# Kernel tuning notes

Hardware: AMD Instinct MI355X
Metric: run time of the kernel (lower is better)

The kernel has to match this reference:

```python
import jax, jax.numpy as jnp
import numpy as np

B = 8192          # sessions
DOCS = 10         # docs per session
NPS = 21          # nodes per session: 1 query + 10 docs + 10 titles
N = B * NPS       # 172032 total nodes
F_IN, F_HID, F_OUT = 171, 256, 128


def _gat_conv(x, src, dst, W, a_src, a_dst, bias, n_nodes):
    # PyG GATConv, heads=1, negative_slope=0.2, self-loops already appended.
    h = x @ W.T                                   # [N, F]
    e = jax.nn.leaky_relu(jnp.take(h @ a_src, src) + jnp.take(h @ a_dst, dst), 0.2)
    m = jax.ops.segment_max(e, dst, num_segments=n_nodes)
    ex = jnp.exp(e - m[dst])
    denom = jax.ops.segment_sum(ex, dst, num_segments=n_nodes)
    alpha = ex / denom[dst]                       # softmax over incoming edges
    out = jax.ops.segment_sum(h[src] * alpha[:, None], dst, num_segments=n_nodes)
    return out + bias


def setup_inputs() -> dict:
    key = jax.random.key(0)
    ks = jax.random.split(key, 20)
    # structured node ids: per session block [q, d0..d9, t0..t9]
    base = jnp.arange(B, dtype=jnp.int64) * NPS
    doc_id = base[:, None] + 1 + jnp.arange(DOCS, dtype=jnp.int64)   # [B,10]
    q = base                                                          # query node = doc_id[:,0]-1
    t = doc_id + DOCS                                                 # title node = doc+10
    qd_s = jnp.repeat(q, DOCS); qd_d = doc_id.reshape(-1)
    dt_s = doc_id.reshape(-1);  dt_d = t.reshape(-1)
    src = jnp.concatenate([qd_s, qd_d, dt_s, dt_d])
    dst = jnp.concatenate([qd_d, qd_s, dt_d, dt_s])
    edge_index = jnp.stack([src, dst])                                # [2, 327680]

    inp = {
        "i": 0,
        "x": jax.random.normal(ks[0], (N, F_IN), jnp.float32),
        "edge_index": edge_index,
        "doc_id": doc_id,
        "click": jax.random.randint(ks[1], (B,), 0, 2),
        "query": jax.random.randint(ks[2], (B,), 0, 6338),
        "docu": jax.random.randint(ks[3], (B, DOCS), 0, 56477),
        "title_id": jax.random.randint(ks[4], (B, DOCS), 0, 56363),
        # embedding tables
        "query_table": jax.random.normal(ks[5], (6338, 160), jnp.float32) * 0.02,
        "doc_table": jax.random.normal(ks[6], (56477, 160), jnp.float32) * 0.02,
        "title_table": jax.random.normal(ks[7], (56363, 160), jnp.float32) * 0.02,
        "pos_table": jax.random.normal(ks[8], (10, 1), jnp.float32) * 0.02,
        "click_table": jax.random.normal(ks[9], (2, 1), jnp.float32) * 0.02,
        # GATConv 1 (171 -> 256)
        "W1": jax.random.normal(ks[10], (F_HID, F_IN), jnp.float32) * (1.0 / np.sqrt(F_IN)),
        "a_src1": jax.random.normal(ks[11], (F_HID,), jnp.float32) * 0.1,
        "a_dst1": jax.random.normal(ks[12], (F_HID,), jnp.float32) * 0.1,
        "b1": jnp.zeros((F_HID,), jnp.float32),
        # GATConv 2 (256 -> 128)
        "W2": jax.random.normal(ks[13], (F_OUT, F_HID), jnp.float32) * (1.0 / np.sqrt(F_HID)),
        "a_src2": jax.random.normal(ks[14], (F_OUT,), jnp.float32) * 0.1,
        "a_dst2": jax.random.normal(ks[15], (F_OUT,), jnp.float32) * 0.1,
        "b2": jnp.zeros((F_OUT,), jnp.float32),
        # head linear (128 -> 1)
        "Wl": jax.random.normal(ks[16], (1, F_OUT), jnp.float32) * (1.0 / np.sqrt(F_OUT)),
        "bl": jnp.zeros((1,), jnp.float32),
    }
    return inp


def reference(i, x, edge_index, doc_id, click, query, docu, title_id,
              query_table, doc_table, title_table, pos_table, click_table,
              W1, a_src1, a_dst1, b1, W2, a_src2, a_dst2, b2, Wl, bl):
    n_nodes = x.shape[0]
    q_emb = query_table[query]          # [B,160]
    d_emb = doc_table[docu]             # [B,10,160]
    t_emb = title_table[title_id]       # [B,10,160]
    pos = pos_table[:, 0]               # [10]  (position_embedding of 0..9)
    clk = click_table[click, 0]         # [B]

    df = doc_id.reshape(-1)             # flat doc node ids [B*10]
    if i == 0:
        x = x.at[doc_id[:, 0] - 1, :160].set(q_emb)
        x = x.at[df, :160].set(d_emb.reshape(-1, 160))
        x = x.at[df, 160].set(jnp.broadcast_to(pos, doc_id.shape).reshape(-1))
        x = x.at[df, 161 + i].set(jnp.broadcast_to(clk[:, None], doc_id.shape).reshape(-1))
        x = x.at[df + 10, :160].set(t_emb.reshape(-1, 160))
    else:
        x = x.at[df, 161 + i].set(jnp.broadcast_to(clk[:, None], doc_id.shape).reshape(-1))

    # add self-loops (PyG GATConv default)
    loop = jnp.arange(n_nodes, dtype=edge_index.dtype)
    src = jnp.concatenate([edge_index[0], loop])
    dst = jnp.concatenate([edge_index[1], loop])

    y = _gat_conv(x, src, dst, W1, a_src1, a_dst1, b1, n_nodes)
    y = jax.nn.relu(y)                  # dropout is identity in eval mode
    hidden_state = _gat_conv(y, src, dst, W2, a_src2, a_dst2, b2, n_nodes)
    y = jax.nn.relu(hidden_state)
    y = jax.nn.sigmoid(y @ Wl.T + bl)   # [N,1]
    return (hidden_state, y, x[:, :171])
```

## Files before the change

### kernel.cpp

```cpp
#include <hip/hip_runtime.h>
#include <cstdint>

#define N_NODES 172032
#define BATCH   8192
#define NPS     21
#define F_IN    171
#define K1P     192
#define F_HID   256
#define F_OUT   128
#define SX_F    (NPS * F_IN)
#define SXP     172
#define SXB     (NPS * K1P)
#define SPB     3
#define NBLK    2731

typedef unsigned short u16;
typedef __attribute__((ext_vector_type(8))) short  bf16x8;
typedef __attribute__((ext_vector_type(4))) float  f32x4;

__device__ inline u16 f2bf(float f) {
    unsigned u = __float_as_uint(f);
    unsigned r = u + 0x7FFFu + ((u >> 16) & 1u);
    return (u16)(r >> 16);
}
__device__ inline float bf2f(u16 h) { return __uint_as_float(((unsigned)h) << 16); }
__device__ inline float lrelu(float v) { return v > 0.f ? v : 0.2f * v; }

__device__ inline int deg_of(int n)  { return n == 0 ? 11 : (n <= 10 ? 3 : 2); }
__device__ inline int edge_base(int n) { return n == 0 ? 0 : (n <= 10 ? 11 + 3*(n-1) : 41 + 2*(n-11)); }
__device__ inline int src_of(int n, int k) {
    if (n == 0)  return k < 10 ? k + 1 : 0;
    if (n <= 10) return k == 0 ? 0 : (k == 1 ? n + 10 : n);
    return k == 0 ? n - 10 : n;
}

__device__ inline float wave_red(float v) {
    for (int off = 32; off; off >>= 1) v += __shfl_down(v, off);
    return v;
}

__global__ __launch_bounds__(256) void build_x(const int* __restrict__ iptr, const float* __restrict__ x,
                        const int* __restrict__ click, const int* __restrict__ query,
                        const int* __restrict__ docu, const int* __restrict__ title_id,
                        const float* __restrict__ qtab, const float* __restrict__ dtab,
                        const float* __restrict__ ttab, const float* __restrict__ ptab,
                        const float* __restrict__ ctab,
                        const float* __restrict__ W1, const float* __restrict__ W2,
                        float* __restrict__ out_x, u16* __restrict__ xb,
                        u16* __restrict__ W1b, u16* __restrict__ W2b)
{
    if (blockIdx.x >= BATCH) {
        int id = (blockIdx.x - BATCH) * 256 + threadIdx.x;
        if (id < 256 * K1P) {
            int r = id / K1P, k = id - r * K1P;
            W1b[id] = (k < F_IN) ? f2bf(W1[r * F_IN + k]) : (u16)0;
        }
        if (id < 128 * 256) W2b[id] = f2bf(W2[id]);
        return;
    }

    __shared__ float sx[NPS * SXP];
    __shared__ int   dz[10], tz[10], s_q;
    __shared__ float s_clk;

    const int s   = blockIdx.x;
    const int tid = threadIdx.x;
    const int i   = iptr[0];
    const long xbase = (long)s * SX_F;

    if (tid < 10)       dz[tid]      = docu[s*10 + tid];
    else if (tid < 20)  tz[tid - 10] = title_id[s*10 + tid - 10];
    else if (tid == 20) s_q          = query[s];
    else if (tid == 21) s_clk        = ctab[click[s]];
    __syncthreads();

    if (i == 0) {
        for (int id = tid; id < NPS * 40; id += 256) {
            int p = id / 40, c4 = (id - p * 40) * 4;
            const float* src;
            if (p == 0)       src = qtab + (long)s_q * 160;
            else if (p <= 10) src = dtab + (long)dz[p-1] * 160;
            else              src = ttab + (long)tz[p-11] * 160;
            *(float4*)(sx + p * SXP + c4) = *(const float4*)(src + c4);
        }
        for (int id = tid; id < NPS * 11; id += 256) {
            int p = id / 11, c = 160 + (id - p * 11);
            float v;
            if (p >= 1 && p <= 10 && c == 160)      v = ptab[p - 1];
            else if (p >= 1 && p <= 10 && c == 161) v = s_clk;
            else                                     v = x[xbase + p * F_IN + c];
            sx[p * SXP + c] = v;
        }
    } else {
        for (int idx = tid; idx < SX_F; idx += 256) {
            int p = idx / F_IN;
            int c = idx - p * F_IN;
            float v = x[xbase + idx];
            if (p >= 1 && p <= 10 && c == 161 + i) v = s_clk;
            sx[p * SXP + c] = v;
        }
    }
    __syncthreads();

    {
        int r    = (int)(xbase & 3);
        int head = (4 - r) & 3;
        if (tid < head) {
            int p = tid / F_IN, c = tid - p * F_IN;
            out_x[xbase + tid] = sx[p * SXP + c];
        }
        int n4 = (SX_F - head) >> 2;
        for (int id = tid; id < n4; id += 256) {
            int o = head + id * 4;
            float4 v;
            {
                int p0 = o / F_IN, c0 = o - p0 * F_IN;
                v.x = sx[p0 * SXP + c0];
                int o1 = o + 1; int p1 = o1 / F_IN, c1 = o1 - p1 * F_IN;
                v.y = sx[p1 * SXP + c1];
                int o2 = o + 2; int p2 = o2 / F_IN, c2 = o2 - p2 * F_IN;
                v.z = sx[p2 * SXP + c2];
                int o3 = o + 3; int p3 = o3 / F_IN, c3 = o3 - p3 * F_IN;
                v.w = sx[p3 * SXP + c3];
            }
            *(float4*)(out_x + xbase + o) = v;
        }
        int done = head + n4 * 4;
        int tail = SX_F - done;
        if (tid < tail) {
            int idx = done + tid;
            int p = idx / F_IN, c = idx - p * F_IN;
            out_x[xbase + idx] = sx[p * SXP + c];
        }
    }

    {
        u16* xbs = xb + (long)s * SXB;
        for (int id = tid; id < SXB / 8; id += 256) {
            int k0 = id * 8;
            int node = k0 / K1P;
            int kk   = k0 - node * K1P;
            union { u16 h[8]; uint4 v; } u;
            #pragma unroll
            for (int j = 0; j < 8; ++j) {
                int c = kk + j;
                u.h[j] = (c < F_IN) ? f2bf(sx[node * SXP + c]) : (u16)0;
            }
            *(uint4*)(xbs + k0) = u.v;
        }
    }
}

__global__ __launch_bounds__(256, 4) void fused1(const u16* __restrict__ xb, const u16* __restrict__ W1b,
                                                 const float* __restrict__ asrc, const float* __restrict__ adst,
                                                 const float* __restrict__ bias, u16* __restrict__ y1b)
{
    constexpr int SA = 200;
    __shared__ __align__(16) u16 hbuf[64 * 256];
    __shared__ float s_part[2][64], d_part[2][64];
    __shared__ float alpha[SPB * 61];

    const int blk = blockIdx.x, tid = threadIdx.x;
    const int s0  = blk * SPB;
    const int nsamp = (s0 + SPB <= BATCH) ? SPB : (BATCH - s0);
    const int nrow  = nsamp * NPS;

    const int lane = tid & 63, w = tid >> 6;
    const int wr = w >> 1, wc = w & 1;
    const int lm = lane & 15, lq = lane >> 4;

    const u16* Ag = xb + (long)s0 * SXB;
    for (int id = tid; id < 64 * 24; id += 256) {
        int row = id / 24, ch = id - row * 24;
        uint4 v;
        if (row < nrow) v = *(const uint4*)(Ag + row * K1P + ch * 8);
        else            v = make_uint4(0u, 0u, 0u, 0u);
        *(uint4*)(hbuf + row * SA + ch * 8) = v;
    }
    __syncthreads();

    f32x4 acc[2][8];
    #pragma unroll
    for (int f = 0; f < 2; ++f)
        #pragma unroll
        for (int g = 0; g < 8; ++g)
            acc[f][g] = (f32x4){0.f, 0.f, 0.f, 0.f};

    #pragma unroll
    for (int kb = 0; kb < K1P / 32; ++kb) {
        int koff = kb * 32 + lq * 8;
        bf16x8 a0 = *(const bf16x8*)(hbuf + (wr*32 +  0 + lm) * SA + koff);
        bf16x8 a1 = *(const bf16x8*)(hbuf + (wr*32 + 16 + lm) * SA + koff);
        #pragma unroll
        for (int g = 0; g < 8; ++g) {
            bf16x8 b = *(const bf16x8*)(W1b + (wc*128 + g*16 + lm) * K1P + koff);
            acc[0][g] = __builtin_amdgcn_mfma_f32_16x16x32_bf16(a0, b, acc[0][g], 0, 0, 0);
            acc[1][g] = __builtin_amdgcn_mfma_f32_16x16x32_bf16(a1, b, acc[1][g], 0, 0, 0);
        }
    }
    __syncthreads();

    u16* h = hbuf;
    float av[8], dv[8];
    #pragma unroll
    for (int g = 0; g < 8; ++g) {
        av[g] = asrc[wc*128 + g*16 + lm];
        dv[g] = adst[wc*128 + g*16 + lm];
    }
    #pragma unroll
    for (int f = 0; f < 2; ++f)
        #pragma unroll
        for (int r = 0; r < 4; ++r) {
            int row = wr*32 + f*16 + lq*4 + r;
            float sp = 0.f, dp = 0.f;
            #pragma unroll
            for (int g = 0; g < 8; ++g) {
                float v = acc[f][g][r];
                h[row * F_HID + wc*128 + g*16 + lm] = f2bf(v);
                sp += v * av[g];
                dp += v * dv[g];
            }
            #pragma unroll
            for (int off = 1; off < 16; off <<= 1) {
                sp += __shfl_xor(sp, off);
                dp += __shfl_xor(dp, off);
            }
            if (lm == 0) { s_part[wc][row] = sp; d_part[wc][row] = dp; }
        }
    __syncthreads();

    if (tid < nrow) {
        int s = tid / NPS, p = tid - s * NPS;
        int deg = deg_of(p), eb = edge_base(p);
        int sb = s * NPS;
        float dn = d_part[0][tid] + d_part[1][tid];
        float e[11];
        float m = -1e30f;
        for (int k = 0; k < deg; ++k) {
            int sn = sb + src_of(p, k);
            e[k] = lrelu(s_part[0][sn] + s_part[1][sn] + dn);
            m = fmaxf(m, e[k]);
        }
        float den = 0.f;
        for (int k = 0; k < deg; ++k) { e[k] = expf(e[k] - m); den += e[k]; }
        float inv = 1.f / den;
        for (int k = 0; k < deg; ++k) alpha[s*61 + eb + k] = e[k] * inv;
    }
    __syncthreads();

    const int c = tid;
    float bc = bias[c];
    for (int s = 0; s < nsamp; ++s) {
        const u16* hs = h + s * NPS * F_HID;
        const float* al = alpha + s * 61;
        u16* outp = y1b + ((long)(s0 + s) * NPS) * F_HID;
        {
            float a = al[10] * bf2f(hs[c]);
            #pragma unroll
            for (int j = 1; j <= 10; ++j) a += al[j-1] * bf2f(hs[j * F_HID + c]);
            outp[c] = f2bf(fmaxf(a + bc, 0.f));
        }
        #pragma unroll
        for (int j = 1; j <= 10; ++j) {
            int eb = 11 + 3*(j-1);
            float a = al[eb]   * bf2f(hs[c])
                    + al[eb+1] * bf2f(hs[(j+10) * F_HID + c])
                    + al[eb+2] * bf2f(hs[j * F_HID + c]);
            outp[j * F_HID + c] = f2bf(fmaxf(a + bc, 0.f));
        }
        #pragma unroll
        for (int j = 1; j <= 10; ++j) {
            int eb = 41 + 2*(j-1);
            float a = al[eb]   * bf2f(hs[j * F_HID + c])
                    + al[eb+1] * bf2f(hs[(10+j) * F_HID + c]);
            outp[(10+j) * F_HID + c] = f2bf(fmaxf(a + bc, 0.f));
        }
    }
}

__global__ __launch_bounds__(256, 4) void fused2(const u16* __restrict__ y1b, const u16* __restrict__ W2b,
                                                 const float* __restrict__ asrc, const float* __restrict__ adst,
                                                 const float* __restrict__ bias,
                                                 const float* __restrict__ Wl, const float* __restrict__ bl,
                                                 float* __restrict__ out_hid, float* __restrict__ out_y)
{
    constexpr int SA = 264;
    __shared__ __align__(16) u16 hbuf[64 * SA];
    __shared__ float s_part[2][64], d_part[2][64];
    __shared__ float alpha[SPB * 61];
    __shared__ float rpart[SPB * NPS][2];

    const int blk = blockIdx.x, tid = threadIdx.x;
    const int s0  = blk * SPB;
    const int nsamp = (s0 + SPB <= BATCH) ? SPB : (BATCH - s0);
    const int nrow  = nsamp * NPS;

    const int lane = tid & 63, w = tid >> 6;
    const int wr = w >> 1, wc = w & 1;
    const int lm = lane & 15, lq = lane >> 4;

    const u16* Ag = y1b + (long)s0 * NPS * F_HID;
    for (int id = tid; id < 64 * 32; id += 256) {
        int row = id >> 5, ch = id & 31;
        uint4 v;
        if (row < nrow) v = *(const uint4*)(Ag + row * F_HID + ch * 8);
        else            v = make_uint4(0u, 0u, 0u, 0u);
        *(uint4*)(hbuf + row * SA + ch * 8) = v;
    }
    __syncthreads();

    f32x4 acc[2][4];
    #pragma unroll
    for (int f = 0; f < 2; ++f)
        #pragma unroll
        for (int g = 0; g < 4; ++g)
            acc[f][g] = (f32x4){0.f, 0.f, 0.f, 0.f};

    #pragma unroll
    for (int kb = 0; kb < F_HID / 32; ++kb) {
        int koff = kb * 32 + lq * 8;
        bf16x8 a0 = *(const bf16x8*)(hbuf + (wr*32 +  0 + lm) * SA + koff);
        bf16x8 a1 = *(const bf16x8*)(hbuf + (wr*32 + 16 + lm) * SA + koff);
        #pragma unroll
        for (int g = 0; g < 4; ++g) {
            bf16x8 b = *(const bf16x8*)(W2b + (wc*64 + g*16 + lm) * F_HID + koff);
            acc[0][g] = __builtin_amdgcn_mfma_f32_16x16x32_bf16(a0, b, acc[0][g], 0, 0, 0);
            acc[1][g] = __builtin_amdgcn_mfma_f32_16x16x32_bf16(a1, b, acc[1][g], 0, 0, 0);
        }
    }
    __syncthreads();

    u16* h2 = hbuf;
    float av[4], dv[4];
    #pragma unroll
    for (int g = 0; g < 4; ++g) {
        av[g] = asrc[wc*64 + g*16 + lm];
        dv[g] = adst[wc*64 + g*16 + lm];
    }
    #pragma unroll
    for (int f = 0; f < 2; ++f)
        #pragma unroll
        for (int r = 0; r < 4; ++r) {
            int row = wr*32 + f*16 + lq*4 + r;
            float sp = 0.f, dp = 0.f;
            #pragma unroll
            for (int g = 0; g < 4; ++g) {
                float v = acc[f][g][r];
                h2[row * F_OUT + wc*64 + g*16 + lm] = f2bf(v);
                sp += v * av[g];
                dp += v * dv[g];
            }
            #pragma unroll
            for (int off = 1; off < 16; off <<= 1) {
                sp += __shfl_xor(sp, off);
                dp += __shfl_xor(dp, off);
            }
            if (lm == 0) { s_part[wc][row] = sp; d_part[wc][row] = dp; }
        }
    __syncthreads();

    if (tid < nrow) {
        int s = tid / NPS, p = tid - s * NPS;
        int deg = deg_of(p), eb = edge_base(p);
        int sb = s * NPS;
        float dn = d_part[0][tid] + d_part[1][tid];
        float e[11];
        float m = -1e30f;
        for (int k = 0; k < deg; ++k) {
            int sn = sb + src_of(p, k);
            e[k] = lrelu(s_part[0][sn] + s_part[1][sn] + dn);
            m = fmaxf(m, e[k]);
        }
        float den = 0.f;
        for (int k = 0; k < deg; ++k) { e[k] = expf(e[k] - m); den += e[k]; }
        float inv = 1.f / den;
        for (int k = 0; k < deg; ++k) alpha[s*61 + eb + k] = e[k] * inv;
    }
    __syncthreads();

    const int c    = tid & 127;
    const int half = tid >> 7;
    float bc = bias[c];
    float wl = Wl[c];
    for (int s = 0; s < nsamp; ++s) {
        const u16* hs = h2 + s * NPS * F_OUT;
        const float* al = alpha + s * 61;
        long gb = (long)(s0 + s) * NPS * F_OUT;
        for (int p = half; p < NPS; p += 2) {
            int deg = deg_of(p), eb = edge_base(p);
            float a = 0.f;
            for (int k = 0; k < deg; ++k) a += al[eb + k] * bf2f(hs[src_of(p,k) * F_OUT + c]);
            float hv = a + bc;
            out_hid[gb + p * F_OUT + c] = hv;
            float rv = wave_red(fmaxf(hv, 0.f) * wl);
            if (lane == 0) rpart[s * NPS + p][w & 1] = rv;
        }
    }
    __syncthreads();

    if (tid < nrow) {
        float v = rpart[tid][0] + rpart[tid][1] + bl[0];
        out_y[(long)s0 * NPS + tid] = 1.f / (1.f + expf(-v));
    }
}

extern "C" void kernel_launch(void* const* d_in, const int* in_sizes, int n_in,
                              void* d_out, int out_size, void* d_ws, size_t ws_size,
                              hipStream_t stream) {
    const int*   ip    = (const int*)  d_in[0];
    const float* x     = (const float*)d_in[1];
    const int*   click = (const int*)  d_in[4];
    const int*   query = (const int*)  d_in[5];
    const int*   docu  = (const int*)  d_in[6];
    const int*   title = (const int*)  d_in[7];
    const float* qtab  = (const float*)d_in[8];
    const float* dtab  = (const float*)d_in[9];
    const float* ttab  = (const float*)d_in[10];
    const float* ptab  = (const float*)d_in[11];
    const float* ctab  = (const float*)d_in[12];
    const float* W1    = (const float*)d_in[13];
    const float* as1   = (const float*)d_in[14];
    const float* ad1   = (const float*)d_in[15];
    const float* b1    = (const float*)d_in[16];
    const float* W2    = (const float*)d_in[17];
    const float* as2   = (const float*)d_in[18];
    const float* ad2   = (const float*)d_in[19];
    const float* b2    = (const float*)d_in[20];
    const float* Wl    = (const float*)d_in[21];
    const float* bl    = (const float*)d_in[22];

    float* out_hid = (float*)d_out;
    float* out_y   = out_hid + (long)N_NODES * F_OUT;
    float* out_x   = out_y + N_NODES;

    u16* xb  = (u16*)d_ws;
    u16* y1b = xb + (long)BATCH * SXB;
    u16* W1b = y1b + (long)N_NODES * F_HID;
    u16* W2b = W1b + 256 * K1P;

    build_x<<<BATCH + 192, 256, 0, stream>>>(ip, x, click, query, docu, title,
                                             qtab, dtab, ttab, ptab, ctab,
                                             W1, W2, out_x, xb, W1b, W2b);
    fused1<<<NBLK, 256, 0, stream>>>(xb, W1b, as1, ad1, b1, y1b);
    fused2<<<NBLK, 256, 0, stream>>>(y1b, W2b, as2, ad2, b2, Wl, bl, out_hid, out_y);
}
```

Measured before the change: 571.1 us.

## Fuse input build and both GAT layers into one per-block kernel

Merges the build_x, fused1 and fused2 kernels into a single kernel that gathers embeddings, writes out_x, converts to bf16 in shared memory, and runs both GAT layers with intermediates kept in LDS. Weight conversion moves to a small separate kernel. This removes the global round trips for the bf16 x buffer and the 256-wide hidden activations, plus two launches. In exchange, LDS use per block rises (two large buffers), launch bounds drop to 2 blocks per CU, and the out_x writes become scalar strided stores instead of float4.

```diff
diff --git a/kernel.cpp b/kernel.cpp
--- a/kernel.cpp
+++ b/kernel.cpp
@@ -9,14 +9,13 @@
 #define F_HID   256
 #define F_OUT   128
 #define SX_F    (NPS * F_IN)
-#define SXP     172
-#define SXB     (NPS * K1P)
 #define SPB     3
 #define NBLK    2731
 
 typedef unsigned short u16;
 typedef __attribute__((ext_vector_type(8))) short  bf16x8;
 typedef __attribute__((ext_vector_type(4))) float  f32x4;
+typedef __attribute__((ext_vector_type(4))) u16    u16x4;
 
 __device__ inline u16 f2bf(float f) {
     unsigned u = __float_as_uint(f);
@@ -39,143 +38,101 @@
     return v;
 }
 
-__global__ __launch_bounds__(256) void build_x(const int* __restrict__ iptr, const float* __restrict__ x,
+__global__ __launch_bounds__(256) void prep_w(const float* __restrict__ W1, const float* __restrict__ W2,
+                                              u16* __restrict__ W1b, u16* __restrict__ W2b)
+{
+    int id = blockIdx.x * 256 + threadIdx.x;
+    if (id < 256 * K1P) {
+        int r = id / K1P, k = id - r * K1P;
+        W1b[id] = (k < F_IN) ? f2bf(W1[r * F_IN + k]) : (u16)0;
+    }
+    if (id < 128 * 256) W2b[id] = f2bf(W2[id]);
+}
+
+__global__ __launch_bounds__(256, 2) void mega(const int* __restrict__ iptr, const float* __restrict__ x,
                         const int* __restrict__ click, const int* __restrict__ query,
                         const int* __restrict__ docu, const int* __restrict__ title_id,
                         const float* __restrict__ qtab, const float* __restrict__ dtab,
                         const float* __restrict__ ttab, const float* __restrict__ ptab,
                         const float* __restrict__ ctab,
-                        const float* __restrict__ W1, const float* __restrict__ W2,
-                        float* __restrict__ out_x, u16* __restrict__ xb,
-                        u16* __restrict__ W1b, u16* __restrict__ W2b)
+                        const u16* __restrict__ W1b, const u16* __restrict__ W2b,
+                        const float* __restrict__ as1, const float* __restrict__ ad1,
+                        const float* __restrict__ b1,
+                        const float* __restrict__ as2, const float* __restrict__ ad2,
+                        const float* __restrict__ b2,
+                        const float* __restrict__ Wl, const float* __restrict__ bl,
+                        float* __restrict__ out_x, float* __restrict__ out_hid,
+                        float* __restrict__ out_y)
 {
-    if (blockIdx.x >= BATCH) {
-        int id = (blockIdx.x - BATCH) * 256 + threadIdx.x;
-        if (id < 256 * K1P) {
-            int r = id / K1P, k = id - r * K1P;
-            W1b[id] = (k < F_IN) ? f2bf(W1[r * F_IN + k]) : (u16)0;
-        }
-        if (id < 128 * 256) W2b[id] = f2bf(W2[id]);
-        return;
-    }
-
-    __shared__ float sx[NPS * SXP];
-    __shared__ int   dz[10], tz[10], s_q;
-    __shared__ float s_clk;
-
-    const int s   = blockIdx.x;
-    const int tid = threadIdx.x;
-    const int i   = iptr[0];
-    const long xbase = (long)s * SX_F;
-
-    if (tid < 10)       dz[tid]      = docu[s*10 + tid];
-    else if (tid < 20)  tz[tid - 10] = title_id[s*10 + tid - 10];
-    else if (tid == 20) s_q          = query[s];
-    else if (tid == 21) s_clk        = ctab[click[s]];
-    __syncthreads();
-
-    if (i == 0) {
-        for (int id = tid; id < NPS * 40; id += 256) {
-            int p = id / 40, c4 = (id - p * 40) * 4;
-            const float* src;
-            if (p == 0)       src = qtab + (long)s_q * 160;
-            else if (p <= 10) src = dtab + (long)dz[p-1] * 160;
-            else              src = ttab + (long)tz[p-11] * 160;
-            *(float4*)(sx + p * SXP + c4) = *(const float4*)(src + c4);
-        }
-        for (int id = tid; id < NPS * 11; id += 256) {
-            int p = id / 11, c = 160 + (id - p * 11);
-            float v;
-            if (p >= 1 && p <= 10 && c == 160)      v = ptab[p - 1];
-            else if (p >= 1 && p <= 10 && c == 161) v = s_clk;
-            else                                     v = x[xbase + p * F_IN + c];
-            sx[p * SXP + c] = v;
-        }
-    } else {
-        for (int idx = tid; idx < SX_F; idx += 256) {
-            int p = idx / F_IN;
-            int c = idx - p * F_IN;
-            float v = x[xbase + idx];
-            if (p >= 1 && p <= 10 && c == 161 + i) v = s_clk;
-            sx[p * SXP + c] = v;
-        }
-    }
-    __syncthreads();
-
-    {
-        int r    = (int)(xbase & 3);
-        int head = (4 - r) & 3;
-        if (tid < head) {
-            int p = tid / F_IN, c = tid - p * F_IN;
-            out_x[xbase + tid] = sx[p * SXP + c];
-        }
-        int n4 = (SX_F - head) >> 2;
-        for (int id = tid; id < n4; id += 256) {
-            int o = head + id * 4;
-            float4 v;
-            {
-                int p0 = o / F_IN, c0 = o - p0 * F_IN;
-                v.x = sx[p0 * SXP + c0];
-                int o1 = o + 1; int p1 = o1 / F_IN, c1 = o1 - p1 * F_IN;
-                v.y = sx[p1 * SXP + c1];
-                int o2 = o + 2; int p2 = o2 / F_IN, c2 = o2 - p2 * F_IN;
-                v.z = sx[p2 * SXP + c2];
-                int o3 = o + 3; int p3 = o3 / F_IN, c3 = o3 - p3 * F_IN;
-                v.w = sx[p3 * SXP + c3];
-            }
-            *(float4*)(out_x + xbase + o) = v;
-        }
-        int done = head + n4 * 4;
-        int tail = SX_F - done;
-        if (tid < tail) {
-            int idx = done + tid;
-            int p = idx / F_IN, c = idx - p * F_IN;
-            out_x[xbase + idx] = sx[p * SXP + c];
-        }
-    }
-
-    {
-        u16* xbs = xb + (long)s * SXB;
-        for (int id = tid; id < SXB / 8; id += 256) {
-            int k0 = id * 8;
-            int node = k0 / K1P;
-            int kk   = k0 - node * K1P;
-            union { u16 h[8]; uint4 v; } u;
-            #pragma unroll
-            for (int j = 0; j < 8; ++j) {
-                int c = kk + j;
-                u.h[j] = (c < F_IN) ? f2bf(sx[node * SXP + c]) : (u16)0;
-            }
-            *(uint4*)(xbs + k0) = u.v;
-        }
-    }
-}
-
-__global__ __launch_bounds__(256, 4) void fused1(const u16* __restrict__ xb, const u16* __restrict__ W1b,
-                                                 const float* __restrict__ asrc, const float* __restrict__ adst,
-                                                 const float* __restrict__ bias, u16* __restrict__ y1b)
-{
-    constexpr int SA = 200;
-    __shared__ __align__(16) u16 hbuf[64 * 256];
+    constexpr int SA1 = 200;
+    constexpr int SA2 = 264;
+    __shared__ __align__(16) u16 R2[64 * SA2];
+    __shared__ __align__(16) u16 R1[64 * F_HID];
     __shared__ float s_part[2][64], d_part[2][64];
     __shared__ float alpha[SPB * 61];
+    __shared__ float rpart[SPB * NPS][2];
+    __shared__ int   dz[SPB][10], tz[SPB][10], sq[SPB];
+    __shared__ float sclk[SPB];
 
     const int blk = blockIdx.x, tid = threadIdx.x;
     const int s0  = blk * SPB;
     const int nsamp = (s0 + SPB <= BATCH) ? SPB : (BATCH - s0);
     const int nrow  = nsamp * NPS;
+    const int i     = iptr[0];
 
     const int lane = tid & 63, w = tid >> 6;
     const int wr = w >> 1, wc = w & 1;
     const int lm = lane & 15, lq = lane >> 4;
 
-    const u16* Ag = xb + (long)s0 * SXB;
-    for (int id = tid; id < 64 * 24; id += 256) {
-        int row = id / 24, ch = id - row * 24;
-        uint4 v;
-        if (row < nrow) v = *(const uint4*)(Ag + row * K1P + ch * 8);
-        else            v = make_uint4(0u, 0u, 0u, 0u);
-        *(uint4*)(hbuf + row * SA + ch * 8) = v;
+    if (tid < 30)      { int ss = tid / 10, j = tid - ss*10;       if (ss < nsamp) dz[ss][j] = docu[(s0+ss)*10 + j]; }
+    else if (tid < 60) { int t = tid - 30; int ss = t/10, j = t - ss*10; if (ss < nsamp) tz[ss][j] = title_id[(s0+ss)*10 + j]; }
+    else if (tid >= 64 && tid < 67) { int ss = tid - 64; if (ss < nsamp) sq[ss]   = query[s0+ss]; }
+    else if (tid >= 67 && tid < 70) { int ss = tid - 67; if (ss < nsamp) sclk[ss] = ctab[click[s0+ss]]; }
+    __syncthreads();
+
+    u16* A1 = R2;
+    if (i == 0) {
+        for (int id = tid; id < nrow * 40; id += 256) {
+            int r = id / 40, c4 = (id - r*40) * 4;
+            int ss = r / NPS, p = r - ss*NPS;
+            const float* srcp;
+            if (p == 0)       srcp = qtab + (long)sq[ss] * 160;
+            else if (p <= 10) srcp = dtab + (long)dz[ss][p-1] * 160;
+            else              srcp = ttab + (long)tz[ss][p-11] * 160;
+            float4 v = *(const float4*)(srcp + c4);
+            float* ox = out_x + (long)(s0+ss) * SX_F + p * F_IN + c4;
+            ox[0] = v.x; ox[1] = v.y; ox[2] = v.z; ox[3] = v.w;
+            u16x4 hv = { f2bf(v.x), f2bf(v.y), f2bf(v.z), f2bf(v.w) };
+            *(u16x4*)(A1 + r * SA1 + c4) = hv;
+        }
+        for (int id = tid; id < nrow * 11; id += 256) {
+            int r = id / 11, c = 160 + (id - r*11);
+            int ss = r / NPS, p = r - ss*NPS;
+            float v;
+            if (p >= 1 && p <= 10 && c == 160)      v = ptab[p-1];
+            else if (p >= 1 && p <= 10 && c == 161) v = sclk[ss];
+            else v = x[(long)(s0+ss) * SX_F + p * F_IN + c];
+            out_x[(long)(s0+ss) * SX_F + p * F_IN + c] = v;
+            A1[r * SA1 + c] = f2bf(v);
+        }
+    } else {
+        const long base0 = (long)s0 * SX_F;
+        for (int idx = tid; idx < nrow * F_IN; idx += 256) {
+            int r = idx / F_IN, c = idx - r * F_IN;
+            int ss = r / NPS, p = r - ss*NPS;
+            float v = x[base0 + idx];
+            if (p >= 1 && p <= 10 && c == 161 + i) v = sclk[ss];
+            out_x[base0 + idx] = v;
+            A1[r * SA1 + c] = f2bf(v);
+        }
+    }
+    for (int id = tid; id < nrow * 21; id += 256) {
+        int r = id / 21, c = F_IN + (id - r*21);
+        A1[r * SA1 + c] = 0;
+    }
+    for (int id = tid; id < (64 - nrow) * 24; id += 256) {
+        int r = nrow + id / 24, ch = id - (id/24)*24;
+        *(uint4*)(A1 + r * SA1 + ch * 8) = make_uint4(0u,0u,0u,0u);
     }
     __syncthreads();
 
@@ -189,8 +146,8 @@
     #pragma unroll
     for (int kb = 0; kb < K1P / 32; ++kb) {
         int koff = kb * 32 + lq * 8;
-        bf16x8 a0 = *(const bf16x8*)(hbuf + (wr*32 +  0 + lm) * SA + koff);
-        bf16x8 a1 = *(const bf16x8*)(hbuf + (wr*32 + 16 + lm) * SA + koff);
+        bf16x8 a0 = *(const bf16x8*)(A1 + (wr*32 +  0 + lm) * SA1 + koff);
+        bf16x8 a1 = *(const bf16x8*)(A1 + (wr*32 + 16 + lm) * SA1 + koff);
         #pragma unroll
         for (int g = 0; g < 8; ++g) {
             bf16x8 b = *(const bf16x8*)(W1b + (wc*128 + g*16 + lm) * K1P + koff);
@@ -198,35 +155,36 @@
             acc[1][g] = __builtin_amdgcn_mfma_f32_16x16x32_bf16(a1, b, acc[1][g], 0, 0, 0);
         }
     }
-    __syncthreads();
-
-    u16* h = hbuf;
-    float av[8], dv[8];
-    #pragma unroll
-    for (int g = 0; g < 8; ++g) {
-        av[g] = asrc[wc*128 + g*16 + lm];
-        dv[g] = adst[wc*128 + g*16 + lm];
-    }
-    #pragma unroll
-    for (int f = 0; f < 2; ++f)
-        #pragma unroll
-        for (int r = 0; r < 4; ++r) {
-            int row = wr*32 + f*16 + lq*4 + r;
-            float sp = 0.f, dp = 0.f;
+
+    u16* h1 = R1;
+    {
+        float av[8], dv[8];
+        #pragma unroll
+        for (int g = 0; g < 8; ++g) {
+            av[g] = as1[wc*128 + g*16 + lm];
+            dv[g] = ad1[wc*128 + g*16 + lm];
+        }
+        #pragma unroll
+        for (int f = 0; f < 2; ++f)
             #pragma unroll
-            for (int g = 0; g < 8; ++g) {
-                float v = acc[f][g][r];
-                h[row * F_HID + wc*128 + g*16 + lm] = f2bf(v);
-                sp += v * av[g];
-                dp += v * dv[g];
-            }
-            #pragma unroll
-            for (int off = 1; off < 16; off <<= 1) {
-                sp += __shfl_xor(sp, off);
-                dp += __shfl_xor(dp, off);
-            }
-            if (lm == 0) { s_part[wc][row] = sp; d_part[wc][row] = dp; }
-        }
+            for (int r = 0; r < 4; ++r) {
+                int row = wr*32 + f*16 + lq*4 + r;
+                float sp = 0.f, dp = 0.f;
+                #pragma unroll
+                for (int g = 0; g < 8; ++g) {
+                    float v = acc[f][g][r];
+                    h1[row * F_HID + wc*128 + g*16 + lm] = f2bf(v);
+                    sp += v * av[g];
+                    dp += v * dv[g];
+                }
+                #pragma unroll
+                for (int off = 1; off < 16; off <<= 1) {
+                    sp += __shfl_xor(sp, off);
+                    dp += __shfl_xor(dp, off);
+                }
+                if (lm == 0) { s_part[wc][row] = sp; d_part[wc][row] = dp; }
+            }
+    }
     __syncthreads();
 
     if (tid < nrow) {
@@ -248,115 +206,88 @@
     }
     __syncthreads();
 
-    const int c = tid;
-    float bc = bias[c];
-    for (int s = 0; s < nsamp; ++s) {
-        const u16* hs = h + s * NPS * F_HID;
-        const float* al = alpha + s * 61;
-        u16* outp = y1b + ((long)(s0 + s) * NPS) * F_HID;
-        {
-            float a = al[10] * bf2f(hs[c]);
+    u16* Y = R2;
+    {
+        const int c = tid;
+        float bc = b1[c];
+        for (int s = 0; s < nsamp; ++s) {
+            const u16* hs = h1 + s * NPS * F_HID;
+            const float* al = alpha + s * 61;
+            u16* yrow = Y + (s * NPS) * SA2;
+            {
+                float a = al[10] * bf2f(hs[c]);
+                #pragma unroll
+                for (int j = 1; j <= 10; ++j) a += al[j-1] * bf2f(hs[j * F_HID + c]);
+                yrow[c] = f2bf(fmaxf(a + bc, 0.f));
+            }
             #pragma unroll
-            for (int j = 1; j <= 10; ++j) a += al[j-1] * bf2f(hs[j * F_HID + c]);
-            outp[c] = f2bf(fmaxf(a + bc, 0.f));
-        }
-        #pragma unroll
-        for (int j = 1; j <= 10; ++j) {
-            int eb = 11 + 3*(j-1);
-            float a = al[eb]   * bf2f(hs[c])
-                    + al[eb+1] * bf2f(hs[(j+10) * F_HID + c])
-                    + al[eb+2] * bf2f(hs[j * F_HID + c]);
-            outp[j * F_HID + c] = f2bf(fmaxf(a + bc, 0.f));
-        }
-        #pragma unroll
-        for (int j = 1; j <= 10; ++j) {
-            int eb = 41 + 2*(j-1);
-            float a = al[eb]   * bf2f(hs[j * F_HID + c])
-                    + al[eb+1] * bf2f(hs[(10+j) * F_HID + c]);
-            outp[(10+j) * F_HID + c] = f2bf(fmaxf(a + bc, 0.f));
-        }
-    }
-}
-
-__global__ __launch_bounds__(256, 4) void fused2(const u16* __restrict__ y1b, const u16* __restrict__ W2b,
-                                                 const float* __restrict__ asrc, const float* __restrict__ adst,
-                                                 const float* __restrict__ bias,
-                                                 const float* __restrict__ Wl, const float* __restrict__ bl,
-                                                 float* __restrict__ out_hid, float* __restrict__ out_y)
-{
-    constexpr int SA = 264;
-    __shared__ __align__(16) u16 hbuf[64 * SA];
-    __shared__ float s_part[2][64], d_part[2][64];
-    __shared__ float alpha[SPB * 61];
-    __shared__ float rpart[SPB * NPS][2];
-
-    const int blk = blockIdx.x, tid = threadIdx.x;
-    const int s0  = blk * SPB;
-    const int nsamp = (s0 + SPB <= BATCH) ? SPB : (BATCH - s0);
-    const int nrow  = nsamp * NPS;
-
-    const int lane = tid & 63, w = tid >> 6;
-    const int wr = w >> 1, wc = w & 1;
-    const int lm = lane & 15, lq = lane >> 4;
-
-    const u16* Ag = y1b + (long)s0 * NPS * F_HID;
-    for (int id = tid; id < 64 * 32; id += 256) {
-        int row = id >> 5, ch = id & 31;
-        uint4 v;
-        if (row < nrow) v = *(const uint4*)(Ag + row * F_HID + ch * 8);
-        else            v = make_uint4(0u, 0u, 0u, 0u);
-        *(uint4*)(hbuf + row * SA + ch * 8) = v;
-    }
-    __syncthreads();
-
-    f32x4 acc[2][4];
+            for (int j = 1; j <= 10; ++j) {
+                int eb = 11 + 3*(j-1);
+                float a = al[eb]   * bf2f(hs[c])
+                        + al[eb+1] * bf2f(hs[(j+10) * F_HID + c])
+                        + al[eb+2] * bf2f(hs[j * F_HID + c]);
+                yrow[j * SA2 + c] = f2bf(fmaxf(a + bc, 0.f));
+            }
+            #pragma unroll
+            for (int j = 1; j <= 10; ++j) {
+                int eb = 41 + 2*(j-1);
+                float a = al[eb]   * bf2f(hs[j * F_HID + c])
+                        + al[eb+1] * bf2f(hs[(10+j) * F_HID + c]);
+                yrow[(10+j) * SA2 + c] = f2bf(fmaxf(a + bc, 0.f));
+            }
+        }
+    }
+    __syncthreads();
+
+    f32x4 acc2[2][4];
     #pragma unroll
     for (int f = 0; f < 2; ++f)
         #pragma unroll
         for (int g = 0; g < 4; ++g)
-            acc[f][g] = (f32x4){0.f, 0.f, 0.f, 0.f};
+            acc2[f][g] = (f32x4){0.f, 0.f, 0.f, 0.f};
 
     #pragma unroll
     for (int kb = 0; kb < F_HID / 32; ++kb) {
         int koff = kb * 32 + lq * 8;
-        bf16x8 a0 = *(const bf16x8*)(hbuf + (wr*32 +  0 + lm) * SA + koff);
-        bf16x8 a1 = *(const bf16x8*)(hbuf + (wr*32 + 16 + lm) * SA + koff);
+        bf16x8 a0 = *(const bf16x8*)(Y + (wr*32 +  0 + lm) * SA2 + koff);
+        bf16x8 a1 = *(const bf16x8*)(Y + (wr*32 + 16 + lm) * SA2 + koff);
         #pragma unroll
         for (int g = 0; g < 4; ++g) {
             bf16x8 b = *(const bf16x8*)(W2b + (wc*64 + g*16 + lm) * F_HID + koff);
-            acc[0][g] = __builtin_amdgcn_mfma_f32_16x16x32_bf16(a0, b, acc[0][g], 0, 0, 0);
-            acc[1][g] = __builtin_amdgcn_mfma_f32_16x16x32_bf16(a1, b, acc[1][g], 0, 0, 0);
-        }
-    }
-    __syncthreads();
-
-    u16* h2 = hbuf;
-    float av[4], dv[4];
-    #pragma unroll
-    for (int g = 0; g < 4; ++g) {
-        av[g] = asrc[wc*64 + g*16 + lm];
-        dv[g] = adst[wc*64 + g*16 + lm];
-    }
-    #pragma unroll
-    for (int f = 0; f < 2; ++f)
-        #pragma unroll
-        for (int r = 0; r < 4; ++r) {
-            int row = wr*32 + f*16 + lq*4 + r;
-            float sp = 0.f, dp = 0.f;
+            acc2[0][g] = __builtin_amdgcn_mfma_f32_16x16x32_bf16(a0, b, acc2[0][g], 0, 0, 0);
+            acc2[1][g] = __builtin_amdgcn_mfma_f32_16x16x32_bf16(a1, b, acc2[1][g], 0, 0, 0);
+        }
+    }
+
+    u16* h2 = R1;
+    {
+        float av[4], dv[4];
+        #pragma unroll
+        for (int g = 0; g < 4; ++g) {
+            av[g] = as2[wc*64 + g*16 + lm];
+            dv[g] = ad2[wc*64 + g*16 + lm];
+        }
+        #pragma unroll
+        for (int f = 0; f < 2; ++f)
             #pragma unroll
-            for (int g = 0; g < 4; ++g) {
-                float v = acc[f][g][r];
-                h2[row * F_OUT + wc*64 + g*16 + lm] = f2bf(v);
-                sp += v * av[g];
-                dp += v * dv[g];
-            }
-            #pragma unroll
-            for (int off = 1; off < 16; off <<= 1) {
-                sp += __shfl_xor(sp, off);
-                dp += __shfl_xor(dp, off);
-            }
-            if (lm == 0) { s_part[wc][row] = sp; d_part[wc][row] = dp; }
-        }
+            for (int r = 0; r < 4; ++r) {
+                int row = wr*32 + f*16 + lq*4 + r;
+                float sp = 0.f, dp = 0.f;
+                #pragma unroll
+                for (int g = 0; g < 4; ++g) {
+                    float v = acc2[f][g][r];
+                    h2[row * F_OUT + wc*64 + g*16 + lm] = f2bf(v);
+                    sp += v * av[g];
+                    dp += v * dv[g];
+                }
+                #pragma unroll
+                for (int off = 1; off < 16; off <<= 1) {
+                    sp += __shfl_xor(sp, off);
+                    dp += __shfl_xor(dp, off);
+                }
+                if (lm == 0) { s_part[wc][row] = sp; d_part[wc][row] = dp; }
+            }
+    }
     __syncthreads();
 
     if (tid < nrow) {
@@ -378,22 +309,24 @@
     }
     __syncthreads();
 
-    const int c    = tid & 127;
-    const int half = tid >> 7;
-    float bc = bias[c];
-    float wl = Wl[c];
-    for (int s = 0; s < nsamp; ++s) {
-        const u16* hs = h2 + s * NPS * F_OUT;
-        const float* al = alpha + s * 61;
-        long gb = (long)(s0 + s) * NPS * F_OUT;
-        for (int p = half; p < NPS; p += 2) {
-            int deg = deg_of(p), eb = edge_base(p);
-            float a = 0.f;
-            for (int k = 0; k < deg; ++k) a += al[eb + k] * bf2f(hs[src_of(p,k) * F_OUT + c]);
-            float hv = a + bc;
-            out_hid[gb + p * F_OUT + c] = hv;
-            float rv = wave_red(fmaxf(hv, 0.f) * wl);
-            if (lane == 0) rpart[s * NPS + p][w & 1] = rv;
+    {
+        const int c    = tid & 127;
+        const int half = tid >> 7;
+        float bc = b2[c];
+        float wl = Wl[c];
+        for (int s = 0; s < nsamp; ++s) {
+            const u16* hs = h2 + s * NPS * F_OUT;
+            const float* al = alpha + s * 61;
+            long gb = (long)(s0 + s) * NPS * F_OUT;
+            for (int p = half; p < NPS; p += 2) {
+                int deg = deg_of(p), eb = edge_base(p);
+                float a = 0.f;
+                for (int k = 0; k < deg; ++k) a += al[eb + k] * bf2f(hs[src_of(p,k) * F_OUT + c]);
+                float hv = a + bc;
+                out_hid[gb + p * F_OUT + c] = hv;
+                float rv = wave_red(fmaxf(hv, 0.f) * wl);
+                if (lane == 0) rpart[s * NPS + p][w & 1] = rv;
+            }
         }
     }
     __syncthreads();
@@ -433,14 +366,12 @@
     float* out_y   = out_hid + (long)N_NODES * F_OUT;
     float* out_x   = out_y + N_NODES;
 
-    u16* xb  = (u16*)d_ws;
-    u16* y1b = xb + (long)BATCH * SXB;
-    u16* W1b = y1b + (long)N_NODES * F_HID;
+    u16* W1b = (u16*)d_ws;
     u16* W2b = W1b + 256 * K1P;
 
-    build_x<<<BATCH + 192, 256, 0, stream>>>(ip, x, click, query, docu, title,
-                                             qtab, dtab, ttab, ptab, ctab,
-                                             W1, W2, out_x, xb, W1b, W2b);
-    fused1<<<NBLK, 256, 0, stream>>>(xb, W1b, as1, ad1, b1, y1b);
-    fused2<<<NBLK, 256, 0, stream>>>(y1b, W2b, as2, ad2, b2, Wl, bl, out_hid, out_y);
-}
+    prep_w<<<192, 256, 0, stream>>>(W1, W2, W1b, W2b);
+    mega<<<NBLK, 256, 0, stream>>>(ip, x, click, query, docu, title,
+                                   qtab, dtab, ttab, ptab, ctab,
+                                   W1b, W2b, as1, ad1, b1, as2, ad2, b2,
+                                   Wl, bl, out_x, out_hid, out_y);
+}
```

New measurement: 624.7 us. 1.09x slower.
